# Performance work log

Measured on AMD Instinct MI355X. Metric: run time of the kernel, lower is better.

The kernel has to match this reference:

```python
import jax, jax.numpy as jnp
import numpy as np

N = 50000      # nodes
E = 800000     # edges
NIN = 512      # input features
NHID = 128     # hidden
NCLS = 64      # classes


def setup_inputs() -> dict:
    key = jax.random.key(0)
    k0, k1, k2, k3 = jax.random.split(key, 4)
    x = jax.random.normal(k0, (N, NIN), dtype=jnp.float32)
    edge_index = jax.random.randint(k1, (2, E), 0, N, dtype=jnp.int64)
    # Glorot-style init for GCNConv linear weights (bias starts at zero in PyG)
    W1 = jax.random.normal(k2, (NIN, NHID), dtype=jnp.float32) * (1.0 / np.sqrt(NIN))
    W2 = jax.random.normal(k3, (NHID, NCLS), dtype=jnp.float32) * (1.0 / np.sqrt(NHID))
    b1 = jnp.zeros((NHID,), dtype=jnp.float32)
    b2 = jnp.zeros((NCLS,), dtype=jnp.float32)
    return {"x": x, "edge_index": edge_index, "W1": W1, "b1": b1, "W2": W2, "b2": b2}


def gcn_conv(x, W, b, src, dst, n):
    """PyG GCNConv: linear transform, then sym-normalized aggregation with self-loops."""
    xw = x @ W                                                  # [n, out]
    ones = jnp.ones(src.shape[0], dtype=xw.dtype)
    deg = jax.ops.segment_sum(ones, dst, num_segments=n) + 1.0  # +1 for self-loop
    dinv = jax.lax.rsqrt(deg)                                   # deg >= 1
    norm = dinv[src] * dinv[dst]                                # [E]
    agg = jax.ops.segment_sum(xw[src] * norm[:, None], dst, num_segments=n)
    agg = agg + (dinv * dinv)[:, None] * xw                     # self-loop messages
    return agg + b


def reference(x, edge_index, W1, b1, W2, b2):
    src, dst = edge_index[0], edge_index[1]
    n = x.shape[0]
    # eval mode: dropout is a no-op; bn is defined but unused in forward
    h = gcn_conv(x, W1, b1, src, dst, n)
    h = jax.nn.relu(h)
    o = gcn_conv(h, W2, b2, src, dst, n)
    return jax.nn.log_softmax(o, axis=1)
```

## Files before the change

### kernel.cpp

```cpp
#include <hip/hip_runtime.h>
#include <hip/hip_bf16.h>
#include <hip/hip_fp16.h>
#include <cstdint>
#include <cstddef>

#define NNODES 50000
#define NEDGES 800000
#define NIN    512
#define NHID   128
#define NCLS   64

#define SCAN_BLK 512
#define SCAN_NB ((NNODES + SCAN_BLK - 1) / SCAN_BLK)

typedef __attribute__((ext_vector_type(8))) short bf16x8;
typedef __attribute__((ext_vector_type(4))) float f32x4;

static __device__ __forceinline__ ushort f2bf(float f) {
    uint32_t u = __float_as_uint(f);
    uint32_t r = (u + 0x7fffu + ((u >> 16) & 1u)) >> 16;
    return (ushort)r;
}
static __device__ __forceinline__ float bf2f(ushort b) {
    return __uint_as_float(((uint32_t)b) << 16);
}
static __device__ __forceinline__ float h2f(ushort u) {
    _Float16 h;
    __builtin_memcpy(&h, &u, 2);
    return (float)h;
}
static __device__ __forceinline__ ushort f2h(float f) {
    _Float16 h = (_Float16)f;
    ushort u;
    __builtin_memcpy(&u, &h, 2);
    return u;
}

static __device__ __forceinline__ unsigned ldsAddr(const void* p) {
    return (unsigned)(size_t)(__attribute__((address_space(3))) const void*)p;
}

__global__ void clear_kernel(int4* __restrict__ p, int n4) {
    int i = blockIdx.x * blockDim.x + threadIdx.x;
    if (i < n4) p[i] = make_int4(0, 0, 0, 0);
}


__global__ void deg_kernel(const int4* __restrict__ dst4, int* __restrict__ deg) {
    int i = blockIdx.x * blockDim.x + threadIdx.x;
    if (i < NEDGES / 4) {
        int4 d = dst4[i];
        atomicAdd(&deg[d.x], 1);
        atomicAdd(&deg[d.y], 1);
        atomicAdd(&deg[d.z], 1);
        atomicAdd(&deg[d.w], 1);
    }
}

__global__ __launch_bounds__(SCAN_BLK) void scan1_kernel(const int* __restrict__ deg,
                                                         int* __restrict__ blkSum,
                                                         float* __restrict__ dinv) {
    int i = blockIdx.x * SCAN_BLK + threadIdx.x;
    int d = (i < NNODES) ? deg[i] : 0;
    if (i < NNODES) dinv[i] = rsqrtf((float)d + 1.0f);
    int v = d;
#pragma unroll
    for (int off = 32; off; off >>= 1) v += __shfl_xor(v, off, 64);
    __shared__ int ws[SCAN_BLK / 64];
    int w = threadIdx.x >> 6;
    if ((threadIdx.x & 63) == 0) ws[w] = v;
    __syncthreads();
    if (threadIdx.x == 0) {
        int s = 0;
#pragma unroll
        for (int k = 0; k < SCAN_BLK / 64; ++k) s += ws[k];
        blkSum[blockIdx.x] = s;
    }
}

__global__ __launch_bounds__(SCAN_BLK) void scan3_kernel(const int* __restrict__ deg,
                                                         const int* __restrict__ blkSum,
                                                         int* __restrict__ rowptr,
                                                         int* __restrict__ cursor) {
    __shared__ int ws[SCAN_BLK / 64];
    __shared__ int boffsh;
    const int lane = threadIdx.x & 63;
    const int w = threadIdx.x >> 6;
    if (w == 0) {
        int accu = 0;
        for (int k = lane; k < blockIdx.x; k += 64) accu += blkSum[k];
#pragma unroll
        for (int off = 32; off; off >>= 1) accu += __shfl_xor(accu, off, 64);
        if (lane == 0) boffsh = accu;
    }
    int i = blockIdx.x * SCAN_BLK + threadIdx.x;
    int v = (i < NNODES) ? deg[i] : 0;
    int inc = v;
#pragma unroll
    for (int off = 1; off < 64; off <<= 1) {
        int o = __shfl_up(inc, off, 64);
        if (lane >= off) inc += o;
    }
    if (lane == 63) ws[w] = inc;
    __syncthreads();
    int wpre = 0;
    for (int k = 0; k < w; ++k) wpre += ws[k];
    if (i < NNODES) {
        int rp = inc - v + wpre + boffsh;
        rowptr[i] = rp;
        cursor[i] = rp;
    }
    if (i == 0) rowptr[NNODES] = NEDGES;
}

__global__ void scatter_kernel(const int* __restrict__ src, const int* __restrict__ dst,
                               int* __restrict__ cursor,
                               const float* __restrict__ dinv, uint* __restrict__ csr) {
    int e = blockIdx.x * blockDim.x + threadIdx.x;
    if (e >= NEDGES) return;
    int d = dst[e];
    int s = src[e];
    int pos = atomicAdd(&cursor[d], 1);
    csr[pos] = (uint)s | ((uint)f2h(dinv[s]) << 16);
}

__global__ void pack_kernel(const float* __restrict__ W1, const float* __restrict__ W2,
                            ushort* __restrict__ p1, ushort* __restrict__ p2) {
    int t = blockIdx.x * blockDim.x + threadIdx.x;
    const int N1 = 16 * 8 * 64 * 8;
    if (t < N1) {
        int j = t & 7;
        int lane = (t >> 3) & 63;
        int cf = (t >> 9) & 7;
        int ks = t >> 12;
        int k = ks * 32 + (lane >> 4) * 8 + j;
        int c = cf * 16 + (lane & 15);
        p1[t] = f2bf(W1[(size_t)k * NHID + c]);
    } else {
        int u = t - N1;
        if (u < 4 * 4 * 64 * 8) {
            int j = u & 7;
            int lane = (u >> 3) & 63;
            int cf = (u >> 9) & 3;
            int ks = u >> 11;
            int k = ks * 32 + (lane >> 4) * 8 + j;
            int c = cf * 16 + (lane & 15);
            p2[u] = f2bf(W2[(size_t)k * NCLS + c]);
        }
    }
}

__global__ __launch_bounds__(256, 2) void gemm1_kernel(const float* __restrict__ A,
                                                       const ushort* __restrict__ packB,
                                                       ushort* __restrict__ C) {
    __shared__ ushort lds[2][64 * 64];
    const int t = threadIdx.x;
    const int lane = t & 63;
    const int w = t >> 6;
    const int rowBase = blockIdx.x * 64;
    const int rl = lane & 15;
    const int kg = lane >> 4;

    bf16x8 bw[16][2];
    {
        const ushort* bbase = packB + (size_t)lane * 8;
#pragma unroll
        for (int ks = 0; ks < 16; ++ks)
#pragma unroll
            for (int q = 0; q < 2; ++q)
                bw[ks][q] = *(const bf16x8*)(bbase + ks * 4096 + (2 * w + q) * 512);
    }

    f32x4 acc[4][2];
#pragma unroll
    for (int rg = 0; rg < 4; ++rg)
#pragma unroll
        for (int q = 0; q < 2; ++q) acc[rg][q] = (f32x4)(0.f);

    const int r0 = t >> 3,         c0 = t & 7;
    const int r1 = (t + 256) >> 3, c1 = (t + 256) & 7;
    int g0 = rowBase + r0; if (g0 >= NNODES) g0 = NNODES - 1;
    int g1 = rowBase + r1; if (g1 >= NNODES) g1 = NNODES - 1;
    const float* ga0 = A + (size_t)g0 * NIN + c0 * 8;
    const float* ga1 = A + (size_t)g1 * NIN + c1 * 8;
    ushort* wd0 = &lds[0][0] + r0 * 64 + ((c0 ^ (r0 & 7)) * 8);
    ushort* wd1 = &lds[0][0] + r1 * 64 + ((c1 ^ (r1 & 7)) * 8);

    auto cvt8 = [](float4 a, float4 b) {
        bf16x8 v;
        v[0] = (short)f2bf(a.x); v[1] = (short)f2bf(a.y);
        v[2] = (short)f2bf(a.z); v[3] = (short)f2bf(a.w);
        v[4] = (short)f2bf(b.x); v[5] = (short)f2bf(b.y);
        v[6] = (short)f2bf(b.z); v[7] = (short)f2bf(b.w);
        return v;
    };

    float4 pend[2][4];
    pend[0][0] = *(const float4*)(ga0);
    pend[0][1] = *(const float4*)(ga0 + 4);
    pend[0][2] = *(const float4*)(ga1);
    pend[0][3] = *(const float4*)(ga1 + 4);
    pend[1][0] = *(const float4*)(ga0 + 64);
    pend[1][1] = *(const float4*)(ga0 + 68);
    pend[1][2] = *(const float4*)(ga1 + 64);
    pend[1][3] = *(const float4*)(ga1 + 68);
    *(bf16x8*)wd0 = cvt8(pend[0][0], pend[0][1]);
    *(bf16x8*)wd1 = cvt8(pend[0][2], pend[0][3]);
    asm volatile("s_waitcnt lgkmcnt(0)" ::: "memory");
    __builtin_amdgcn_s_barrier();

#pragma unroll
    for (int tch = 0; tch < 8; ++tch) {
        const int cur = tch & 1;
        if (tch + 2 < 8) {
            pend[cur][0] = *(const float4*)(ga0 + (tch + 2) * 64);
            pend[cur][1] = *(const float4*)(ga0 + (tch + 2) * 64 + 4);
            pend[cur][2] = *(const float4*)(ga1 + (tch + 2) * 64);
            pend[cur][3] = *(const float4*)(ga1 + (tch + 2) * 64 + 4);
            __builtin_amdgcn_sched_barrier(0);
        }
        const unsigned lbase = ldsAddr(&lds[cur][0]);
#pragma unroll
        for (int ks = 0; ks < 2; ++ks) {
            bf16x8 af0, af1, af2, af3;
            const unsigned sw = (unsigned)(((ks * 4 + kg) ^ (rl & 7)) * 16);
            const unsigned a0 = lbase + (unsigned)((0 * 16 + rl) * 128) + sw;
            const unsigned a1 = lbase + (unsigned)((1 * 16 + rl) * 128) + sw;
            const unsigned a2 = lbase + (unsigned)((2 * 16 + rl) * 128) + sw;
            const unsigned a3 = lbase + (unsigned)((3 * 16 + rl) * 128) + sw;
            asm volatile("ds_read_b128 %0, %1" : "=&v"(af0) : "v"(a0));
            asm volatile("ds_read_b128 %0, %1" : "=&v"(af1) : "v"(a1));
            asm volatile("ds_read_b128 %0, %1" : "=&v"(af2) : "v"(a2));
            asm volatile("ds_read_b128 %0, %1" : "=&v"(af3) : "v"(a3));
            asm volatile("s_waitcnt lgkmcnt(0)" ::: "memory");
            __builtin_amdgcn_sched_barrier(0);
            const int kq = tch * 2 + ks;
            acc[0][0] = __builtin_amdgcn_mfma_f32_16x16x32_bf16(af0, bw[kq][0], acc[0][0], 0, 0, 0);
            acc[0][1] = __builtin_amdgcn_mfma_f32_16x16x32_bf16(af0, bw[kq][1], acc[0][1], 0, 0, 0);
            acc[1][0] = __builtin_amdgcn_mfma_f32_16x16x32_bf16(af1, bw[kq][0], acc[1][0], 0, 0, 0);
            acc[1][1] = __builtin_amdgcn_mfma_f32_16x16x32_bf16(af1, bw[kq][1], acc[1][1], 0, 0, 0);
            acc[2][0] = __builtin_amdgcn_mfma_f32_16x16x32_bf16(af2, bw[kq][0], acc[2][0], 0, 0, 0);
            acc[2][1] = __builtin_amdgcn_mfma_f32_16x16x32_bf16(af2, bw[kq][1], acc[2][1], 0, 0, 0);
            acc[3][0] = __builtin_amdgcn_mfma_f32_16x16x32_bf16(af3, bw[kq][0], acc[3][0], 0, 0, 0);
            acc[3][1] = __builtin_amdgcn_mfma_f32_16x16x32_bf16(af3, bw[kq][1], acc[3][1], 0, 0, 0);
        }
        if (tch + 1 < 8) {
            const int nxt = cur ^ 1;
            *(bf16x8*)(wd0 + nxt * 4096) = cvt8(pend[nxt][0], pend[nxt][1]);
            *(bf16x8*)(wd1 + nxt * 4096) = cvt8(pend[nxt][2], pend[nxt][3]);
        }
        asm volatile("s_waitcnt lgkmcnt(0)" ::: "memory");
        __builtin_amdgcn_s_barrier();
    }

#pragma unroll
    for (int rg = 0; rg < 4; ++rg)
#pragma unroll
        for (int q = 0; q < 2; ++q)
#pragma unroll
            for (int j = 0; j < 4; ++j) {
                int rr = rowBase + rg * 16 + kg * 4 + j;
                if (rr < NNODES)
                    C[(size_t)rr * NHID + (2 * w + q) * 16 + rl] = f2bf(acc[rg][q][j]);
            }
}

__global__ __launch_bounds__(256) void gemm2_kernel(const ushort* __restrict__ A,
                                                    const ushort* __restrict__ packB,
                                                    ushort* __restrict__ C) {
    int wid = (blockIdx.x * blockDim.x + threadIdx.x) >> 6;
    int lane = threadIdx.x & 63;
    int rowBase = wid * 16;
    if (rowBase >= NNODES) return;
    int rl = lane & 15;
    int kg = lane >> 4;
    const ushort* ap = A + (size_t)(rowBase + rl) * NHID + kg * 8;

    f32x4 acc[4];
#pragma unroll
    for (int cf = 0; cf < 4; ++cf) acc[cf] = (f32x4)(0.f);

#pragma unroll
    for (int ks = 0; ks < 4; ++ks) {
        bf16x8 af = *(const bf16x8*)(ap + ks * 32);
        const ushort* bp = packB + ((size_t)(ks * 4) * 64 + lane) * 8;
#pragma unroll
        for (int cf = 0; cf < 4; ++cf) {
            bf16x8 bf = *(const bf16x8*)(bp + (size_t)cf * 512);
            acc[cf] = __builtin_amdgcn_mfma_f32_16x16x32_bf16(af, bf, acc[cf], 0, 0, 0);
        }
    }
#pragma unroll
    for (int cf = 0; cf < 4; ++cf)
#pragma unroll
        for (int j = 0; j < 4; ++j)
            C[(size_t)(rowBase + kg * 4 + j) * NCLS + cf * 16 + rl] = f2bf(acc[cf][j]);
}

__global__ __launch_bounds__(256) void agg1_kernel(const ushort* __restrict__ xw,
                                                   const int* __restrict__ rowptr,
                                                   const uint* __restrict__ csr,
                                                   const float* __restrict__ dinv,
                                                   const float* __restrict__ b1,
                                                   ushort* __restrict__ h) {
    int wid = (blockIdx.x * blockDim.x + threadIdx.x) >> 6;
    int lane = threadIdx.x & 63;
    if (wid >= NNODES) return;
    int beg = rowptr[wid], end = rowptr[wid + 1];
    float a0 = 0.f, a1 = 0.f, a2 = 0.f, a3 = 0.f;
    int j = beg;
    for (; j + 16 <= end; j += 16) {
        uint e[16];
#pragma unroll
        for (int q = 0; q < 16; ++q) e[q] = csr[j + q];
        uint v[16];
#pragma unroll
        for (int q = 0; q < 16; ++q)
            v[q] = *(const uint*)&xw[(size_t)(e[q] & 0xffffu) * NHID + lane * 2];
#pragma unroll
        for (int q = 0; q < 8; ++q) {
            float wq = h2f((ushort)(e[q] >> 16));
            a0 += wq * __uint_as_float(v[q] << 16);
            a1 += wq * __uint_as_float(v[q] & 0xffff0000u);
        }
#pragma unroll
        for (int q = 8; q < 16; ++q) {
            float wq = h2f((ushort)(e[q] >> 16));
            a2 += wq * __uint_as_float(v[q] << 16);
            a3 += wq * __uint_as_float(v[q] & 0xffff0000u);
        }
    }
    for (; j + 4 <= end; j += 4) {
        uint e[4];
#pragma unroll
        for (int q = 0; q < 4; ++q) e[q] = csr[j + q];
        uint v[4];
#pragma unroll
        for (int q = 0; q < 4; ++q)
            v[q] = *(const uint*)&xw[(size_t)(e[q] & 0xffffu) * NHID + lane * 2];
#pragma unroll
        for (int q = 0; q < 4; ++q) {
            float wq = h2f((ushort)(e[q] >> 16));
            a0 += wq * __uint_as_float(v[q] << 16);
            a1 += wq * __uint_as_float(v[q] & 0xffff0000u);
        }
    }
    for (; j < end; ++j) {
        uint e = csr[j];
        float wq = h2f((ushort)(e >> 16));
        uint v = *(const uint*)&xw[(size_t)(e & 0xffffu) * NHID + lane * 2];
        a0 += wq * __uint_as_float(v << 16);
        a1 += wq * __uint_as_float(v & 0xffff0000u);
    }
    a0 += a2; a1 += a3;
    float di = dinv[wid];
    float sl = di * di;
    uint xv = *(const uint*)&xw[(size_t)wid * NHID + lane * 2];
    float2 bv = *(const float2*)&b1[lane * 2];
    float r0 = di * a0 + sl * __uint_as_float(xv << 16) + bv.x;
    float r1 = di * a1 + sl * __uint_as_float(xv & 0xffff0000u) + bv.y;
    uint o = (uint)f2bf(fmaxf(r0, 0.f)) | ((uint)f2bf(fmaxf(r1, 0.f)) << 16);
    *(uint*)&h[(size_t)wid * NHID + lane * 2] = o;
}

__global__ __launch_bounds__(256) void agg2_kernel(const ushort* __restrict__ xw,
                                                   const int* __restrict__ rowptr,
                                                   const uint* __restrict__ csr,
                                                   const float* __restrict__ dinv,
                                                   const float* __restrict__ b2,
                                                   float* __restrict__ out) {
    int wid = (blockIdx.x * blockDim.x + threadIdx.x) >> 6;
    int lane = threadIdx.x & 63;
    if (wid >= NNODES) return;
    int beg = rowptr[wid], end = rowptr[wid + 1];
    float a = 0.f, b = 0.f;
    int j = beg;
    for (; j + 16 <= end; j += 16) {
        uint e[16];
#pragma unroll
        for (int q = 0; q < 16; ++q) e[q] = csr[j + q];
        float v[16];
#pragma unroll
        for (int q = 0; q < 16; ++q)
            v[q] = bf2f(xw[(size_t)(e[q] & 0xffffu) * NCLS + lane]);
#pragma unroll
        for (int q = 0; q < 8; ++q) a += h2f((ushort)(e[q] >> 16)) * v[q];
#pragma unroll
        for (int q = 8; q < 16; ++q) b += h2f((ushort)(e[q] >> 16)) * v[q];
    }
    for (; j + 4 <= end; j += 4) {
        uint e[4];
#pragma unroll
        for (int q = 0; q < 4; ++q) e[q] = csr[j + q];
        float v[4];
#pragma unroll
        for (int q = 0; q < 4; ++q)
            v[q] = bf2f(xw[(size_t)(e[q] & 0xffffu) * NCLS + lane]);
#pragma unroll
        for (int q = 0; q < 4; ++q) a += h2f((ushort)(e[q] >> 16)) * v[q];
    }
    for (; j < end; ++j) {
        uint e = csr[j];
        a += h2f((ushort)(e >> 16)) * bf2f(xw[(size_t)(e & 0xffffu) * NCLS + lane]);
    }
    a += b;
    float di = dinv[wid];
    float o = di * a + di * di * bf2f(xw[(size_t)wid * NCLS + lane]) + b2[lane];
    float m = o;
#pragma unroll
    for (int off = 32; off; off >>= 1) m = fmaxf(m, __shfl_xor(m, off, 64));
    float ex = __expf(o - m);
    float ssum = ex;
#pragma unroll
    for (int off = 32; off; off >>= 1) ssum += __shfl_xor(ssum, off, 64);
    out[(size_t)wid * NCLS + lane] = (o - m) - __logf(ssum);
}


extern "C" void kernel_launch(void* const* d_in, const int* in_sizes, int n_in,
                              void* d_out, int out_size, void* d_ws, size_t ws_size,
                              hipStream_t stream) {
    const float* x  = (const float*)d_in[0];
    const int*   ei = (const int*)d_in[1];
    const int*   src = ei;
    const int*   dst = ei + NEDGES;
    const float* W1 = (const float*)d_in[2];
    const float* b1 = (const float*)d_in[3];
    const float* W2 = (const float*)d_in[4];
    const float* b2 = (const float*)d_in[5];
    float* out = (float*)d_out;

    char* w = (char*)d_ws;
    auto alloc = [&](size_t bytes) {
        char* p = w;
        w += (bytes + 255) & ~(size_t)255;
        return p;
    };
    int*    deg    = (int*)alloc(NNODES * 4);
    int*    cursor = (int*)alloc(NNODES * 4);
    int*    rowptr = (int*)alloc((NNODES + 1) * 4);
    int*    blkSum = (int*)alloc(SCAN_NB * 4);
    uint*   csr    = (uint*)alloc((size_t)NEDGES * 4);
    float*  dinv   = (float*)alloc(NNODES * 4);
    ushort* pack1  = (ushort*)alloc((size_t)16 * 8 * 64 * 8 * 2);
    ushort* pack2  = (ushort*)alloc((size_t)4 * 4 * 64 * 8 * 2);
    ushort* xw1    = (ushort*)alloc((size_t)NNODES * NHID * 2);
    ushort* h      = (ushort*)alloc((size_t)NNODES * NHID * 2);
    ushort* xw2    = (ushort*)alloc((size_t)NNODES * NCLS * 2);

    const int n4 = (NNODES + 3) / 4;
    clear_kernel<<<(n4 + 255) / 256, 256, 0, stream>>>((int4*)deg, n4);

    deg_kernel<<<(NEDGES / 4 + 255) / 256, 256, 0, stream>>>((const int4*)dst, deg);
    scan1_kernel<<<SCAN_NB, SCAN_BLK, 0, stream>>>(deg, blkSum, dinv);
    scan3_kernel<<<SCAN_NB, SCAN_BLK, 0, stream>>>(deg, blkSum, rowptr, cursor);
    scatter_kernel<<<(NEDGES + 255) / 256, 256, 0, stream>>>(src, dst, cursor, dinv, csr);

    pack_kernel<<<(16 * 8 * 64 * 8 + 4 * 4 * 64 * 8 + 255) / 256, 256, 0, stream>>>(W1, W2, pack1, pack2);

    gemm1_kernel<<<(NNODES + 63) / 64, 256, 0, stream>>>(x, pack1, xw1);
    agg1_kernel<<<(NNODES * 64 + 255) / 256, 256, 0, stream>>>(xw1, rowptr, csr, dinv, b1, h);

    gemm2_kernel<<<(NNODES / 16 + 3) / 4, 256, 0, stream>>>(h, pack2, xw2);
    agg2_kernel<<<(NNODES * 64 + 255) / 256, 256, 0, stream>>>(xw2, rowptr, csr, dinv, b2, out);
}
```

Baseline: 192.6 us.

## Fuse weight packing into degree pass, CSR scatter into GEMM1, and agg1 with GEMM2

Three fusions cut the launch count and an intermediate buffer. The weight-pack work runs as extra blocks of the degree-counting kernel, and the CSR scatter runs as extra blocks of the first GEMM. Layer-1 aggregation now writes the ReLU'd hidden rows into LDS, and the same block multiplies them by W2 with MFMA, so the h buffer no longer goes through global memory. The cost is that agg1g2 blocks must wait at a barrier for all four waves' variable-degree rows, and the GEMM1 kernel carries the scatter path's launch-bound constraints.

```diff
diff --git a/kernel.cpp b/kernel.cpp
--- a/kernel.cpp
+++ b/kernel.cpp
@@ -13,6 +13,13 @@
 #define SCAN_BLK 512
 #define SCAN_NB ((NNODES + SCAN_BLK - 1) / SCAN_BLK)
 
+#define G1_BLOCKS ((NNODES + 63) / 64)
+#define SCAT_BLOCKS ((NEDGES + 255) / 256)
+#define DEG_BLOCKS ((NEDGES / 4 + 255) / 256)
+#define PACK_N1 (16 * 8 * 64 * 8)
+#define PACK_N2 (4 * 4 * 64 * 8)
+#define PACK_BLOCKS ((PACK_N1 + PACK_N2) / 256)
+
 typedef __attribute__((ext_vector_type(8))) short bf16x8;
 typedef __attribute__((ext_vector_type(4))) float f32x4;
 
@@ -45,15 +52,40 @@
     if (i < n4) p[i] = make_int4(0, 0, 0, 0);
 }
 
-
-__global__ void deg_kernel(const int4* __restrict__ dst4, int* __restrict__ deg) {
-    int i = blockIdx.x * blockDim.x + threadIdx.x;
-    if (i < NEDGES / 4) {
-        int4 d = dst4[i];
-        atomicAdd(&deg[d.x], 1);
-        atomicAdd(&deg[d.y], 1);
-        atomicAdd(&deg[d.z], 1);
-        atomicAdd(&deg[d.w], 1);
+__global__ void deg_pack_kernel(const int4* __restrict__ dst4, int* __restrict__ deg,
+                                const float* __restrict__ W1, const float* __restrict__ W2,
+                                ushort* __restrict__ p1, ushort* __restrict__ p2) {
+    if (blockIdx.x < DEG_BLOCKS) {
+        int i = blockIdx.x * 256 + threadIdx.x;
+        if (i < NEDGES / 4) {
+            int4 d = dst4[i];
+            atomicAdd(&deg[d.x], 1);
+            atomicAdd(&deg[d.y], 1);
+            atomicAdd(&deg[d.z], 1);
+            atomicAdd(&deg[d.w], 1);
+        }
+    } else {
+        int t = (blockIdx.x - DEG_BLOCKS) * 256 + threadIdx.x;
+        if (t < PACK_N1) {
+            int j = t & 7;
+            int lane = (t >> 3) & 63;
+            int cf = (t >> 9) & 7;
+            int ks = t >> 12;
+            int k = ks * 32 + (lane >> 4) * 8 + j;
+            int c = cf * 16 + (lane & 15);
+            p1[t] = f2bf(W1[(size_t)k * NHID + c]);
+        } else {
+            int u = t - PACK_N1;
+            if (u < PACK_N2) {
+                int j = u & 7;
+                int lane = (u >> 3) & 63;
+                int cf = (u >> 9) & 3;
+                int ks = u >> 11;
+                int k = ks * 32 + (lane >> 4) * 8 + j;
+                int c = cf * 16 + (lane & 15);
+                p2[u] = f2bf(W2[(size_t)k * NCLS + c]);
+            }
+        }
     }
 }
 
@@ -113,46 +145,22 @@
     if (i == 0) rowptr[NNODES] = NEDGES;
 }
 
-__global__ void scatter_kernel(const int* __restrict__ src, const int* __restrict__ dst,
-                               int* __restrict__ cursor,
-                               const float* __restrict__ dinv, uint* __restrict__ csr) {
-    int e = blockIdx.x * blockDim.x + threadIdx.x;
-    if (e >= NEDGES) return;
-    int d = dst[e];
-    int s = src[e];
-    int pos = atomicAdd(&cursor[d], 1);
-    csr[pos] = (uint)s | ((uint)f2h(dinv[s]) << 16);
-}
-
-__global__ void pack_kernel(const float* __restrict__ W1, const float* __restrict__ W2,
-                            ushort* __restrict__ p1, ushort* __restrict__ p2) {
-    int t = blockIdx.x * blockDim.x + threadIdx.x;
-    const int N1 = 16 * 8 * 64 * 8;
-    if (t < N1) {
-        int j = t & 7;
-        int lane = (t >> 3) & 63;
-        int cf = (t >> 9) & 7;
-        int ks = t >> 12;
-        int k = ks * 32 + (lane >> 4) * 8 + j;
-        int c = cf * 16 + (lane & 15);
-        p1[t] = f2bf(W1[(size_t)k * NHID + c]);
-    } else {
-        int u = t - N1;
-        if (u < 4 * 4 * 64 * 8) {
-            int j = u & 7;
-            int lane = (u >> 3) & 63;
-            int cf = (u >> 9) & 3;
-            int ks = u >> 11;
-            int k = ks * 32 + (lane >> 4) * 8 + j;
-            int c = cf * 16 + (lane & 15);
-            p2[u] = f2bf(W2[(size_t)k * NCLS + c]);
-        }
-    }
-}
-
-__global__ __launch_bounds__(256, 2) void gemm1_kernel(const float* __restrict__ A,
-                                                       const ushort* __restrict__ packB,
-                                                       ushort* __restrict__ C) {
+__global__ __launch_bounds__(256, 2) void gemm1_scatter_kernel(
+        const float* __restrict__ A, const ushort* __restrict__ packB,
+        ushort* __restrict__ C,
+        const int* __restrict__ src, const int* __restrict__ dst,
+        int* __restrict__ cursor, const float* __restrict__ dinv,
+        uint* __restrict__ csr) {
+    if (blockIdx.x >= G1_BLOCKS) {
+        int e = (blockIdx.x - G1_BLOCKS) * 256 + threadIdx.x;
+        if (e < NEDGES) {
+            int d = dst[e];
+            int s = src[e];
+            int pos = atomicAdd(&cursor[d], 1);
+            csr[pos] = (uint)s | ((uint)f2h(dinv[s]) << 16);
+        }
+        return;
+    }
     __shared__ ushort lds[2][64 * 64];
     const int t = threadIdx.x;
     const int lane = t & 63;
@@ -265,102 +273,96 @@
             }
 }
 
-__global__ __launch_bounds__(256) void gemm2_kernel(const ushort* __restrict__ A,
-                                                    const ushort* __restrict__ packB,
-                                                    ushort* __restrict__ C) {
-    int wid = (blockIdx.x * blockDim.x + threadIdx.x) >> 6;
-    int lane = threadIdx.x & 63;
-    int rowBase = wid * 16;
-    if (rowBase >= NNODES) return;
-    int rl = lane & 15;
-    int kg = lane >> 4;
-    const ushort* ap = A + (size_t)(rowBase + rl) * NHID + kg * 8;
-
-    f32x4 acc[4];
-#pragma unroll
-    for (int cf = 0; cf < 4; ++cf) acc[cf] = (f32x4)(0.f);
-
+__global__ __launch_bounds__(256) void agg1g2_kernel(const ushort* __restrict__ xw,
+                                                     const int* __restrict__ rowptr,
+                                                     const uint* __restrict__ csr,
+                                                     const float* __restrict__ dinv,
+                                                     const float* __restrict__ b1,
+                                                     const ushort* __restrict__ pack2,
+                                                     ushort* __restrict__ xw2) {
+    __shared__ ushort hlds[16][136];
+    const int t = threadIdx.x;
+    const int lane = t & 63;
+    const int w = t >> 6;
+    const int rowBase = blockIdx.x * 16;
+
+    bf16x8 bfr[4];
+#pragma unroll
+    for (int ks = 0; ks < 4; ++ks)
+        bfr[ks] = *(const bf16x8*)(pack2 + ((size_t)(ks * 4 + w) * 64 + lane) * 8);
+
+    for (int i = 0; i < 4; ++i) {
+        const int nl = w * 4 + i;
+        const int wid = rowBase + nl;
+        int beg = rowptr[wid], end = rowptr[wid + 1];
+        float a0 = 0.f, a1 = 0.f, a2 = 0.f, a3 = 0.f;
+        int j = beg;
+        for (; j + 16 <= end; j += 16) {
+            uint e[16];
+#pragma unroll
+            for (int q = 0; q < 16; ++q) e[q] = csr[j + q];
+            uint v[16];
+#pragma unroll
+            for (int q = 0; q < 16; ++q)
+                v[q] = *(const uint*)&xw[(size_t)(e[q] & 0xffffu) * NHID + lane * 2];
+#pragma unroll
+            for (int q = 0; q < 8; ++q) {
+                float wq = h2f((ushort)(e[q] >> 16));
+                a0 += wq * __uint_as_float(v[q] << 16);
+                a1 += wq * __uint_as_float(v[q] & 0xffff0000u);
+            }
+#pragma unroll
+            for (int q = 8; q < 16; ++q) {
+                float wq = h2f((ushort)(e[q] >> 16));
+                a2 += wq * __uint_as_float(v[q] << 16);
+                a3 += wq * __uint_as_float(v[q] & 0xffff0000u);
+            }
+        }
+        for (; j + 4 <= end; j += 4) {
+            uint e[4];
+#pragma unroll
+            for (int q = 0; q < 4; ++q) e[q] = csr[j + q];
+            uint v[4];
+#pragma unroll
+            for (int q = 0; q < 4; ++q)
+                v[q] = *(const uint*)&xw[(size_t)(e[q] & 0xffffu) * NHID + lane * 2];
+#pragma unroll
+            for (int q = 0; q < 4; ++q) {
+                float wq = h2f((ushort)(e[q] >> 16));
+                a0 += wq * __uint_as_float(v[q] << 16);
+                a1 += wq * __uint_as_float(v[q] & 0xffff0000u);
+            }
+        }
+        for (; j < end; ++j) {
+            uint e = csr[j];
+            float wq = h2f((ushort)(e >> 16));
+            uint v = *(const uint*)&xw[(size_t)(e & 0xffffu) * NHID + lane * 2];
+            a0 += wq * __uint_as_float(v << 16);
+            a1 += wq * __uint_as_float(v & 0xffff0000u);
+        }
+        a0 += a2; a1 += a3;
+        float di = dinv[wid];
+        float sl = di * di;
+        uint xv = *(const uint*)&xw[(size_t)wid * NHID + lane * 2];
+        float2 bv = *(const float2*)&b1[lane * 2];
+        float r0 = di * a0 + sl * __uint_as_float(xv << 16) + bv.x;
+        float r1 = di * a1 + sl * __uint_as_float(xv & 0xffff0000u) + bv.y;
+        uint o = (uint)f2bf(fmaxf(r0, 0.f)) | ((uint)f2bf(fmaxf(r1, 0.f)) << 16);
+        *(uint*)&hlds[nl][lane * 2] = o;
+    }
+    __syncthreads();
+
+    const int rl = lane & 15;
+    const int kg = lane >> 4;
+    f32x4 acc = (f32x4)(0.f);
 #pragma unroll
     for (int ks = 0; ks < 4; ++ks) {
-        bf16x8 af = *(const bf16x8*)(ap + ks * 32);
-        const ushort* bp = packB + ((size_t)(ks * 4) * 64 + lane) * 8;
-#pragma unroll
-        for (int cf = 0; cf < 4; ++cf) {
-            bf16x8 bf = *(const bf16x8*)(bp + (size_t)cf * 512);
-            acc[cf] = __builtin_amdgcn_mfma_f32_16x16x32_bf16(af, bf, acc[cf], 0, 0, 0);
-        }
-    }
-#pragma unroll
-    for (int cf = 0; cf < 4; ++cf)
-#pragma unroll
-        for (int j = 0; j < 4; ++j)
-            C[(size_t)(rowBase + kg * 4 + j) * NCLS + cf * 16 + rl] = f2bf(acc[cf][j]);
-}
-
-__global__ __launch_bounds__(256) void agg1_kernel(const ushort* __restrict__ xw,
-                                                   const int* __restrict__ rowptr,
-                                                   const uint* __restrict__ csr,
-                                                   const float* __restrict__ dinv,
-                                                   const float* __restrict__ b1,
-                                                   ushort* __restrict__ h) {
-    int wid = (blockIdx.x * blockDim.x + threadIdx.x) >> 6;
-    int lane = threadIdx.x & 63;
-    if (wid >= NNODES) return;
-    int beg = rowptr[wid], end = rowptr[wid + 1];
-    float a0 = 0.f, a1 = 0.f, a2 = 0.f, a3 = 0.f;
-    int j = beg;
-    for (; j + 16 <= end; j += 16) {
-        uint e[16];
-#pragma unroll
-        for (int q = 0; q < 16; ++q) e[q] = csr[j + q];
-        uint v[16];
-#pragma unroll
-        for (int q = 0; q < 16; ++q)
-            v[q] = *(const uint*)&xw[(size_t)(e[q] & 0xffffu) * NHID + lane * 2];
-#pragma unroll
-        for (int q = 0; q < 8; ++q) {
-            float wq = h2f((ushort)(e[q] >> 16));
-            a0 += wq * __uint_as_float(v[q] << 16);
-            a1 += wq * __uint_as_float(v[q] & 0xffff0000u);
-        }
-#pragma unroll
-        for (int q = 8; q < 16; ++q) {
-            float wq = h2f((ushort)(e[q] >> 16));
-            a2 += wq * __uint_as_float(v[q] << 16);
-            a3 += wq * __uint_as_float(v[q] & 0xffff0000u);
-        }
-    }
-    for (; j + 4 <= end; j += 4) {
-        uint e[4];
-#pragma unroll
-        for (int q = 0; q < 4; ++q) e[q] = csr[j + q];
-        uint v[4];
-#pragma unroll
-        for (int q = 0; q < 4; ++q)
-            v[q] = *(const uint*)&xw[(size_t)(e[q] & 0xffffu) * NHID + lane * 2];
-#pragma unroll
-        for (int q = 0; q < 4; ++q) {
-            float wq = h2f((ushort)(e[q] >> 16));
-            a0 += wq * __uint_as_float(v[q] << 16);
-            a1 += wq * __uint_as_float(v[q] & 0xffff0000u);
-        }
-    }
-    for (; j < end; ++j) {
-        uint e = csr[j];
-        float wq = h2f((ushort)(e >> 16));
-        uint v = *(const uint*)&xw[(size_t)(e & 0xffffu) * NHID + lane * 2];
-        a0 += wq * __uint_as_float(v << 16);
-        a1 += wq * __uint_as_float(v & 0xffff0000u);
-    }
-    a0 += a2; a1 += a3;
-    float di = dinv[wid];
-    float sl = di * di;
-    uint xv = *(const uint*)&xw[(size_t)wid * NHID + lane * 2];
-    float2 bv = *(const float2*)&b1[lane * 2];
-    float r0 = di * a0 + sl * __uint_as_float(xv << 16) + bv.x;
-    float r1 = di * a1 + sl * __uint_as_float(xv & 0xffff0000u) + bv.y;
-    uint o = (uint)f2bf(fmaxf(r0, 0.f)) | ((uint)f2bf(fmaxf(r1, 0.f)) << 16);
-    *(uint*)&h[(size_t)wid * NHID + lane * 2] = o;
+        bf16x8 af = *(const bf16x8*)&hlds[rl][ks * 32 + kg * 8];
+        acc = __builtin_amdgcn_mfma_f32_16x16x32_bf16(af, bfr[ks], acc, 0, 0, 0);
+    }
+#pragma unroll
+    for (int j = 0; j < 4; ++j)
+        xw2[(size_t)(rowBase + kg * 4 + j) * NCLS + w * 16 + rl] = f2bf(acc[j]);
 }
 
 __global__ __launch_bounds__(256) void agg2_kernel(const ushort* __restrict__ xw,
@@ -442,25 +444,23 @@
     int*    blkSum = (int*)alloc(SCAN_NB * 4);
     uint*   csr    = (uint*)alloc((size_t)NEDGES * 4);
     float*  dinv   = (float*)alloc(NNODES * 4);
-    ushort* pack1  = (ushort*)alloc((size_t)16 * 8 * 64 * 8 * 2);
-    ushort* pack2  = (ushort*)alloc((size_t)4 * 4 * 64 * 8 * 2);
+    ushort* pack1  = (ushort*)alloc((size_t)PACK_N1 * 2);
+    ushort* pack2  = (ushort*)alloc((size_t)PACK_N2 * 2);
     ushort* xw1    = (ushort*)alloc((size_t)NNODES * NHID * 2);
-    ushort* h      = (ushort*)alloc((size_t)NNODES * NHID * 2);
     ushort* xw2    = (ushort*)alloc((size_t)NNODES * NCLS * 2);
 
     const int n4 = (NNODES + 3) / 4;
     clear_kernel<<<(n4 + 255) / 256, 256, 0, stream>>>((int4*)deg, n4);
 
-    deg_kernel<<<(NEDGES / 4 + 255) / 256, 256, 0, stream>>>((const int4*)dst, deg);
+    deg_pack_kernel<<<DEG_BLOCKS + PACK_BLOCKS, 256, 0, stream>>>(
+        (const int4*)dst, deg, W1, W2, pack1, pack2);
     scan1_kernel<<<SCAN_NB, SCAN_BLK, 0, stream>>>(deg, blkSum, dinv);
     scan3_kernel<<<SCAN_NB, SCAN_BLK, 0, stream>>>(deg, blkSum, rowptr, cursor);
-    scatter_kernel<<<(NEDGES + 255) / 256, 256, 0, stream>>>(src, dst, cursor, dinv, csr);
-
-    pack_kernel<<<(16 * 8 * 64 * 8 + 4 * 4 * 64 * 8 + 255) / 256, 256, 0, stream>>>(W1, W2, pack1, pack2);
-
-    gemm1_kernel<<<(NNODES + 63) / 64, 256, 0, stream>>>(x, pack1, xw1);
-    agg1_kernel<<<(NNODES * 64 + 255) / 256, 256, 0, stream>>>(xw1, rowptr, csr, dinv, b1, h);
-
-    gemm2_kernel<<<(NNODES / 16 + 3) / 4, 256, 0, stream>>>(h, pack2, xw2);
+
+    gemm1_scatter_kernel<<<G1_BLOCKS + SCAT_BLOCKS, 256, 0, stream>>>(
+        x, pack1, xw1, src, dst, cursor, dinv, csr);
+
+    agg1g2_kernel<<<NNODES / 16, 256, 0, stream>>>(xw1, rowptr, csr, dinv, b1, pack2, xw2);
+
     agg2_kernel<<<(NNODES * 64 + 255) / 256, 256, 0, stream>>>(xw2, rowptr, csr, dinv, b2, out);
 }
```

After: 198.8 us. 1.03x slower.
